# Kernel tuning notes

Measured on AMD Instinct MI355X. Metric: run time of the kernel, lower is better.

The kernel has to match this reference:

```python
import jax, jax.numpy as jnp
import numpy as np

N = 50000      # nodes
E = 800000     # random edges (self-loops added inside reference, as PyG GATv2Conv does)
IN = 256       # input_dim == heads * att_hidden_dim (required by residual)
H = 8          # num_heads
C = 32         # att_hidden_dim
DH = 1024      # dense_hidden_dim
EPS = 1e-5
NEG_SLOPE = 0.2


def setup_inputs() -> dict:
    key = jax.random.key(0)
    ks = jax.random.split(key, 8)
    s = 0.05
    return {
        "x": jax.random.normal(ks[0], (N, IN), jnp.float32),
        "edge_index": jax.random.randint(ks[1], (2, E), 0, N, dtype=jnp.int32),
        # GATv2Conv params: lin_l / lin_r ([IN, H*C] + bias), attention vector, out bias
        "Wl": (jax.random.normal(ks[2], (IN, H * C), jnp.float32) * s),
        "bl": jnp.zeros((H * C,), jnp.float32),
        "Wr": (jax.random.normal(ks[3], (IN, H * C), jnp.float32) * s),
        "br": jnp.zeros((H * C,), jnp.float32),
        "att": (jax.random.normal(ks[4], (H, C), jnp.float32) * s),
        "b_gat": jnp.zeros((H * C,), jnp.float32),
        # LayerNorm 1 (PyG graph-mode) affine params
        "g1": jnp.ones((H * C,), jnp.float32),
        "be1": jnp.zeros((H * C,), jnp.float32),
        # MLP: dense_2 (H*C -> DH), dense_3 (DH -> IN)
        "W2": (jax.random.normal(ks[5], (H * C, DH), jnp.float32) * s),
        "b2": jnp.zeros((DH,), jnp.float32),
        "W3": (jax.random.normal(ks[6], (DH, IN), jnp.float32) * s),
        "b3": jnp.zeros((IN,), jnp.float32),
        # LayerNorm 3 affine params
        "g3": jnp.ones((IN,), jnp.float32),
        "be3": jnp.zeros((IN,), jnp.float32),
    }


def graph_layernorm(x, g, b):
    # torch_geometric.nn.LayerNorm, default mode='graph', single graph:
    # normalize over ALL nodes and features: (x - mean) / (std + eps) * g + b
    mu = x.mean()
    xc = x - mu
    std = jnp.sqrt((xc * xc).mean())
    return (xc / (std + EPS)) * g + b


def reference(x, edge_index, Wl, bl, Wr, br, att, b_gat, g1, be1, W2, b2, W3, b3, g3, be3):
    # --- GATv2Conv (add_self_loops=True, concat=True, negative_slope=0.2) ---
    loops = jnp.arange(N, dtype=edge_index.dtype)
    src = jnp.concatenate([edge_index[0], loops])  # message sources j
    dst = jnp.concatenate([edge_index[1], loops])  # message targets i

    xl = (x @ Wl + bl).reshape(N, H, C)  # source-side transform (lin_l)
    xr = (x @ Wr + br).reshape(N, H, C)  # target-side transform (lin_r)

    # per-edge GATv2 attention: leaky_relu(x_l[j] + x_r[i]) . att
    e = jax.nn.leaky_relu(xl[src] + xr[dst], NEG_SLOPE)   # [E+N, H, C]
    logits = jnp.einsum('ehc,hc->eh', e, att)             # [E+N, H]

    # segment softmax over incoming edges of each target node
    m = jax.ops.segment_max(logits, dst, num_segments=N)  # [N, H]
    p = jnp.exp(logits - m[dst])
    denom = jax.ops.segment_sum(p, dst, num_segments=N)   # [N, H]
    alpha = p / denom[dst]                                # [E+N, H]

    # scatter-add weighted source features
    agg = jax.ops.segment_sum(alpha[:, :, None] * xl[src], dst, num_segments=N)
    gat_out = agg.reshape(N, H * C) + b_gat               # concat heads + bias

    # --- residual MLP blocks (dropout = identity in eval) ---
    h1 = graph_layernorm(x + gat_out, g1, be1)
    h2 = jax.nn.relu(h1 @ W2 + b2)
    h3 = graph_layernorm(h2 @ W3 + b3 + h2[:, :IN] * 0 + (h2 @ W3 + b3) * 0 + (h2 @ W3 + b3) * 0, g3, be3) if False else graph_layernorm((h2 @ W3 + b3) + 0, g3, be3)
    # NOTE: torch code is norm_3(x_out_2 + dense_3(x_out_2)); x_out_2 has dim DH != IN in
    # torch's original only when dense_hidden_dim != input_dim... faithful version below:
    h3 = graph_layernorm(h2 @ W3 + b3, g3, be3)
    return h3
```

## Files before the change

### kernel.cpp

```cpp
#include <hip/hip_runtime.h>
#include <hip/hip_bf16.h>

#define HC 256
#define DHID 1024
#define LN_EPS 1e-5f
#define NSLOT 1024

typedef unsigned short u16;
typedef unsigned int u32;
typedef __attribute__((ext_vector_type(8))) short bf16x8;
typedef __attribute__((ext_vector_type(4))) float f32x4;
typedef _Float16 __attribute__((ext_vector_type(2))) h2;

__device__ __forceinline__ float bf2f(u16 u) {
  union { u32 i; float f; } v; v.i = ((u32)u) << 16; return v.f;
}
__device__ __forceinline__ u16 f2bf(float f) {
  union { float f; u32 i; } v; v.f = f;
  u32 r = v.i + 0x7fffu + ((v.i >> 16) & 1u);
  return (u16)(r >> 16);
}
__device__ __forceinline__ u16 f2h(float f) {
  union { _Float16 h; u16 u; } v; v.h = (_Float16)f; return v.u;
}
__device__ __forceinline__ float dot2(h2 a, h2 b, float c) {
  return __builtin_amdgcn_fdot2(a, b, c, false);
}
__device__ __forceinline__ void gload16(const u16* g, u16* ldsbase, int byteoff) {
  __builtin_amdgcn_global_load_lds(
      (const __attribute__((address_space(1))) void*)g,
      (__attribute__((address_space(3))) void*)((char*)ldsbase + byteoff),
      16, 0, 0);
}

template<bool RELU, int OMODE>
__global__ __launch_bounds__(512, 4) void gemm_mfma(
    const u16* __restrict__ Ab, const u16* __restrict__ BT,
    const float* __restrict__ bias,
    void* __restrict__ outp, double* __restrict__ sl,
    int M, int K, int NB)
{
  __shared__ __align__(16) u16 Asm[256 * 64];
  __shared__ __align__(16) u16 Bsm[128 * 64];
  const int tid = threadIdx.x;
  const int wid = tid >> 6, lane = tid & 63;
  const int rowBase = blockIdx.x * 256;
  const int colBase = blockIdx.y * 128;
  const int wr = (wid >> 1) * 64, wc = (wid & 1) * 64;
  const int ccol = lane & 15, g = lane >> 4;
  f32x4 acc[4][4] = {};
  const int nt = K >> 6;

  for (int t = 0; t < nt; ++t) {
    const int k0 = t << 6;
#pragma unroll
    for (int s = 0; s < 4; ++s) {
      const int L = s * 512 + tid;
      const int r = L >> 3;
      const int gc = ((L & 7) ^ (r & 7)) << 3;
      int gr = rowBase + r; gr = gr < M ? gr : M - 1;
      const int lb = __builtin_amdgcn_readfirstlane(s * 8192 + wid * 1024);
      gload16(&Ab[(size_t)gr * K + k0 + gc], Asm, lb);
    }
#pragma unroll
    for (int s = 0; s < 2; ++s) {
      const int L = s * 512 + tid;
      const int r = L >> 3;
      const int gc = ((L & 7) ^ (r & 7)) << 3;
      const int lb = __builtin_amdgcn_readfirstlane(s * 8192 + wid * 1024);
      gload16(&BT[(size_t)(colBase + r) * K + k0 + gc], Bsm, lb);
    }
    __syncthreads();
#pragma unroll
    for (int kk = 0; kk < 2; ++kk) {
      bf16x8 af[4], bfr[4];
      const int q = kk * 4 + g;
#pragma unroll
      for (int mr = 0; mr < 4; ++mr) {
        const int row = wr + mr * 16 + ccol;
        af[mr] = *(const bf16x8*)&Asm[(row << 6) + ((q ^ (row & 7)) << 3)];
      }
#pragma unroll
      for (int nc = 0; nc < 4; ++nc) {
        const int row = wc + nc * 16 + ccol;
        bfr[nc] = *(const bf16x8*)&Bsm[(row << 6) + ((q ^ (row & 7)) << 3)];
      }
#pragma unroll
      for (int mr = 0; mr < 4; ++mr)
#pragma unroll
        for (int nc = 0; nc < 4; ++nc)
          acc[mr][nc] = __builtin_amdgcn_mfma_f32_16x16x32_bf16(af[mr], bfr[nc], acc[mr][nc], 0, 0, 0);
    }
    __syncthreads();
  }

  u16* ob = (u16*)outp;
  float* of = (float*)outp;
  const int crow = g * 4;
  float s1 = 0.f, s2 = 0.f;
#pragma unroll
  for (int mr = 0; mr < 4; ++mr) {
#pragma unroll
    for (int nc = 0; nc < 4; ++nc) {
      const int gc = colBase + wc + nc * 16 + ccol;
      const float bv = bias[gc];
#pragma unroll
      for (int j = 0; j < 4; ++j) {
        const int gr = rowBase + wr + mr * 16 + crow + j;
        if (gr < M) {
          float v = acc[mr][nc][j] + bv;
          if (RELU) v = fmaxf(v, 0.f);
          if (OMODE == 1) {
            ob[(size_t)gr * NB + gc] = f2bf(v);
          } else if (OMODE == 2) {
            ob[(size_t)gr * NB + gc] = f2h(v);
          } else {
            of[(size_t)gr * NB + gc] = v;
            s1 += v; s2 += v * v;
          }
        }
      }
    }
  }
  if (OMODE == 0) {
#pragma unroll
    for (int d = 1; d < 64; d <<= 1) {
      s1 += __shfl_xor(s1, d);
      s2 += __shfl_xor(s2, d);
    }
    if (lane == 0) {
      int slot = ((blockIdx.x + blockIdx.y * 397) * 8 + wid) & (NSLOT - 1);
      atomicAdd(&sl[slot * 2 + 0], (double)s1);
      atomicAdd(&sl[slot * 2 + 1], (double)s2);
    }
  }
}

__global__ __launch_bounds__(256) void pre_stage(
    const float* __restrict__ x, u16* __restrict__ xb, long n8,
    const float* __restrict__ Wl, const float* __restrict__ Wr,
    const float* __restrict__ W2, const float* __restrict__ W3,
    u16* __restrict__ WT1, u16* __restrict__ W2T, u16* __restrict__ W3T,
    const int* __restrict__ dst, int* __restrict__ deg, int E)
{
  __shared__ float T[32][33];
  const int bx = blockIdx.x;
  if (bx < 2048) {
    for (long i = (long)bx * 256 + threadIdx.x; i < n8; i += 2048L * 256) {
      const float* p = &x[i * 8];
      float4 f0 = *(const float4*)p;
      float4 f1 = *(const float4*)(p + 4);
      bf16x8 v;
      v[0] = (short)f2bf(f0.x); v[1] = (short)f2bf(f0.y);
      v[2] = (short)f2bf(f0.z); v[3] = (short)f2bf(f0.w);
      v[4] = (short)f2bf(f1.x); v[5] = (short)f2bf(f1.y);
      v[6] = (short)f2bf(f1.z); v[7] = (short)f2bf(f1.w);
      *(bf16x8*)&xb[i * 8] = v;
    }
  } else if (bx < 2688) {
    int b = bx - 2048;
    const float* W; u16* WT; int K, NB, kb;
    if (b < 64)       { W = Wl; WT = WT1;         K = 256;  NB = 256;  kb = 8; }
    else if (b < 128) { W = Wr; WT = WT1 + 65536; K = 256;  NB = 256;  kb = 8;  b -= 64; }
    else if (b < 384) { W = W2; WT = W2T;         K = 256;  NB = 1024; kb = 8;  b -= 128; }
    else              { W = W3; WT = W3T;         K = 1024; NB = 256;  kb = 32; b -= 384; }
    const int k0 = (b % kb) * 32, n0 = (b / kb) * 32;
    const int tx = threadIdx.x & 31, ty = threadIdx.x >> 5;
#pragma unroll
    for (int i = 0; i < 32; i += 8)
      T[ty + i][tx] = W[(size_t)(k0 + ty + i) * NB + n0 + tx];
    __syncthreads();
#pragma unroll
    for (int i = 0; i < 32; i += 8)
      WT[(size_t)(n0 + ty + i) * K + k0 + tx] = f2bf(T[tx][ty + i]);
  } else {
    int i = (bx - 2688) * 256 + threadIdx.x;
    if (i < E) atomicAdd(&deg[dst[i]], 1);
  }
}

__global__ __launch_bounds__(256) void w2fold(
    u16* __restrict__ W2T, const float* __restrict__ A1c,
    const float* __restrict__ b2, const float* __restrict__ B1c,
    const float* __restrict__ W2, float* __restrict__ bias2p)
{
  const int bx = blockIdx.x;
  if (bx < 128) {
    const int i = bx * 256 + threadIdx.x;
    const int kb = (i & 31) << 3;
    bf16x8 v = *(bf16x8*)&W2T[(size_t)i * 8];
    float4 a0 = *(const float4*)&A1c[kb];
    float4 a1 = *(const float4*)&A1c[kb + 4];
    bf16x8 w;
    w[0] = (short)f2bf(bf2f((u16)v[0]) * a0.x);
    w[1] = (short)f2bf(bf2f((u16)v[1]) * a0.y);
    w[2] = (short)f2bf(bf2f((u16)v[2]) * a0.z);
    w[3] = (short)f2bf(bf2f((u16)v[3]) * a0.w);
    w[4] = (short)f2bf(bf2f((u16)v[4]) * a1.x);
    w[5] = (short)f2bf(bf2f((u16)v[5]) * a1.y);
    w[6] = (short)f2bf(bf2f((u16)v[6]) * a1.z);
    w[7] = (short)f2bf(bf2f((u16)v[7]) * a1.w);
    *(bf16x8*)&W2T[(size_t)i * 8] = w;
  } else {
    const int n = (bx - 128) * 256 + threadIdx.x;
    if (n < DHID) {
      float s = b2[n];
      for (int k = 0; k < HC; ++k) s = fmaf(B1c[k], W2[(size_t)k * DHID + n], s);
      bias2p[n] = s;
    }
  }
}

__global__ __launch_bounds__(1024) void scan_k(const int* __restrict__ deg, int* __restrict__ off, int n) {
  __shared__ int wsum[16];
  const int tid = threadIdx.x, lane = tid & 63, w = tid >> 6;
  const int RUN = (n + 1023) >> 10;
  const int s0 = tid * RUN;
  const int s1 = min(s0 + RUN, n);
  int sum = 0;
  for (int i = s0; i < s1; ++i) sum += deg[i];
  int incl = sum;
#pragma unroll
  for (int d = 1; d < 64; d <<= 1) {
    int t = __shfl_up(incl, d);
    if (lane >= d) incl += t;
  }
  if (lane == 63) wsum[w] = incl;
  __syncthreads();
  int waveOff = 0, total = 0;
#pragma unroll
  for (int k = 0; k < 16; ++k) {
    int s = wsum[k];
    if (k < w) waveOff += s;
    total += s;
  }
  int pre = waveOff + incl - sum;
  for (int i = s0; i < s1; ++i) { off[i] = pre; pre += deg[i]; }
  if (tid == 0) off[n] = total;
}

__global__ void fill_csr(const int* __restrict__ src, const int* __restrict__ dst,
                         const int* __restrict__ off, int* __restrict__ cur,
                         int* __restrict__ csr, int E) {
  int i = blockIdx.x * blockDim.x + threadIdx.x;
  if (i < E) {
    int d = dst[i];
    int pos = off[d] + atomicAdd(&cur[d], 1);
    csr[pos] = src[i] << 10;
  }
}

__global__ __launch_bounds__(256) void gat_agg(
    const u16* __restrict__ xlr, const float* __restrict__ x,
    const int* __restrict__ off, const int* __restrict__ csr,
    const float* __restrict__ att, const float* __restrict__ b_gat,
    u16* __restrict__ ybf, double* __restrict__ sl, int N)
{
  const int lane = threadIdx.x & 63;
  const int node = blockIdx.x * 4 + (threadIdx.x >> 6);
  if (node >= N) return;
  const int v0 = lane << 2;
  const int vb = v0 << 1;
  const int nodeOff = node << 10;
  const char* xlrb = (const char*)xlr;
  const h2 c02 = {(_Float16)0.2f, (_Float16)0.2f};
  h2 att01, att23;
  {
    float4 attf = *(const float4*)&att[v0];
    att01 = (h2){(_Float16)attf.x, (_Float16)attf.y};
    att23 = (h2){(_Float16)attf.z, (_Float16)attf.w};
  }
  h2 xr01, xr23;
  {
    uint2 ux = *(const uint2*)(xlrb + nodeOff + 512 + vb);
    xr01 = __builtin_bit_cast(h2, ux.x);
    xr23 = __builtin_bit_cast(h2, ux.y);
  }
  float m0, d_run = 1.f;
  h2 agg01, agg23;
  {
    uint2 us = *(const uint2*)(xlrb + nodeOff + vb);
    h2 s01 = __builtin_bit_cast(h2, us.x);
    h2 s23 = __builtin_bit_cast(h2, us.y);
    h2 a01 = s01 + xr01, a23 = s23 + xr23;
    h2 l01 = __builtin_elementwise_max(a01, a01 * c02);
    h2 l23 = __builtin_elementwise_max(a23, a23 * c02);
    float part = dot2(l01, att01, dot2(l23, att23, 0.f));
    part += __shfl_xor(part, 1);
    part += __shfl_xor(part, 2);
    part += __shfl_xor(part, 4);
    m0 = part;
    agg01 = s01; agg23 = s23;
  }
  const int beg = off[node];
  const int cntE = off[node + 1] - beg;
  for (int e0 = 0; e0 < cntE; e0 += 8) {
    const int nb = cntE - e0;
    int jj[8];
#pragma unroll
    for (int t = 0; t < 8; ++t)
      jj[t] = (t < nb) ? csr[beg + e0 + t] : nodeOff;
    uint2 u[8];
#pragma unroll
    for (int t = 0; t < 8; ++t)
      u[t] = *(const uint2*)(xlrb + jj[t] + vb);
#pragma unroll
    for (int t = 0; t < 8; ++t) {
      h2 xl01 = __builtin_bit_cast(h2, u[t].x);
      h2 xl23 = __builtin_bit_cast(h2, u[t].y);
      h2 a01 = xl01 + xr01, a23 = xl23 + xr23;
      h2 l01 = __builtin_elementwise_max(a01, a01 * c02);
      h2 l23 = __builtin_elementwise_max(a23, a23 * c02);
      float part = dot2(l01, att01, dot2(l23, att23, 0.f));
      part += __shfl_xor(part, 1);
      part += __shfl_xor(part, 2);
      part += __shfl_xor(part, 4);
      float p = (t < nb) ? __expf(part - m0) : 0.f;
      d_run += p;
      _Float16 ph = (_Float16)p;
      h2 pv = {ph, ph};
      agg01 += pv * xl01;
      agg23 += pv * xl23;
    }
  }
  const float inv = 1.f / d_run;
  float xv[4], bg[4];
  *(float4*)xv = *(const float4*)&x[(size_t)node * HC + v0];
  *(float4*)bg = *(const float4*)&b_gat[v0];
  float s1, s2;
  ushort4 ov;
  {
    float v0f = fmaf((float)agg01.x, inv, bg[0]) + xv[0];
    float v1f = fmaf((float)agg01.y, inv, bg[1]) + xv[1];
    float v2f = fmaf((float)agg23.x, inv, bg[2]) + xv[2];
    float v3f = fmaf((float)agg23.y, inv, bg[3]) + xv[3];
    s1 = v0f + v1f + v2f + v3f;
    s2 = v0f * v0f + v1f * v1f + v2f * v2f + v3f * v3f;
    ov.x = f2bf(v0f); ov.y = f2bf(v1f); ov.z = f2bf(v2f); ov.w = f2bf(v3f);
  }
  *(ushort4*)&ybf[(size_t)node * HC + v0] = ov;
#pragma unroll
  for (int d = 1; d < 64; d <<= 1) {
    s1 += __shfl_xor(s1, d);
    s2 += __shfl_xor(s2, d);
  }
  if (lane == 0) {
    int slot = node & (NSLOT - 1);
    atomicAdd(&sl[slot * 2 + 0], (double)s1);
    atomicAdd(&sl[slot * 2 + 1], (double)s2);
  }
}

__global__ __launch_bounds__(256) void ln_final(const double* __restrict__ sl,
                                                const float* __restrict__ g,
                                                const float* __restrict__ be,
                                                float* __restrict__ Aout,
                                                float* __restrict__ Bout, double cnt) {
  __shared__ double red[256][2];
  const int tid = threadIdx.x;
  double s1 = 0.0, s2 = 0.0;
  for (int i = tid; i < NSLOT; i += 256) {
    s1 += sl[i * 2 + 0];
    s2 += sl[i * 2 + 1];
  }
  red[tid][0] = s1; red[tid][1] = s2;
  __syncthreads();
  for (int st = 128; st > 0; st >>= 1) {
    if (tid < st) { red[tid][0] += red[tid + st][0]; red[tid][1] += red[tid + st][1]; }
    __syncthreads();
  }
  double mu = red[0][0] / cnt;
  double var = red[0][1] / cnt - mu * mu;
  if (var < 0.0) var = 0.0;
  float sc = (float)(1.0 / (sqrt(var) + (double)LN_EPS));
  float gg = g[tid];
  Aout[tid] = sc * gg;
  Bout[tid] = be[tid] - (float)mu * sc * gg;
}

__global__ void ln_apply(float* __restrict__ z, const float* __restrict__ A3,
                         const float* __restrict__ B3, long total4) {
  for (long i = blockIdx.x * (long)blockDim.x + threadIdx.x; i < total4;
       i += (long)gridDim.x * blockDim.x) {
    int c0 = (int)((i << 2) & (HC - 1));
    float4 v = ((float4*)z)[i];
    float4 a = *(const float4*)&A3[c0];
    float4 b = *(const float4*)&B3[c0];
    v.x = fmaf(v.x, a.x, b.x);
    v.y = fmaf(v.y, a.y, b.y);
    v.z = fmaf(v.z, a.z, b.z);
    v.w = fmaf(v.w, a.w, b.w);
    ((float4*)z)[i] = v;
  }
}

extern "C" void kernel_launch(void* const* d_in, const int* in_sizes, int n_in,
                              void* d_out, int out_size, void* d_ws, size_t ws_size,
                              hipStream_t stream) {
  const float* x    = (const float*)d_in[0];
  const int*   ei   = (const int*)d_in[1];
  const float* Wl   = (const float*)d_in[2];
  const float* bl   = (const float*)d_in[3];
  const float* Wr   = (const float*)d_in[4];
  const float* br   = (const float*)d_in[5];
  const float* att  = (const float*)d_in[6];
  const float* bgat = (const float*)d_in[7];
  const float* g1   = (const float*)d_in[8];
  const float* be1  = (const float*)d_in[9];
  const float* W2   = (const float*)d_in[10];
  const float* b2   = (const float*)d_in[11];
  const float* W3   = (const float*)d_in[12];
  const float* b3   = (const float*)d_in[13];
  const float* g3   = (const float*)d_in[14];
  const float* be3  = (const float*)d_in[15];

  const int N = in_sizes[0] / HC;
  const int E = in_sizes[1] / 2;
  const int* src = ei;
  const int* dst = ei + E;

  char* ws = (char*)d_ws;
  size_t o = 0;
  double* sl1 = (double*)(ws + o); o += (size_t)NSLOT * 16;
  double* sl3 = (double*)(ws + o); o += (size_t)NSLOT * 16;
  float* A1 = (float*)(ws + o); o += HC * 4;
  float* B1 = (float*)(ws + o); o += HC * 4;
  float* A3 = (float*)(ws + o); o += HC * 4;
  float* B3 = (float*)(ws + o); o += HC * 4;
  float* biascat = (float*)(ws + o); o += 512 * 4;
  float* bias2p = (float*)(ws + o); o += DHID * 4;
  u16* WT1 = (u16*)(ws + o); o += (size_t)512 * HC * 2;
  u16* W2T = (u16*)(ws + o); o += (size_t)DHID * HC * 2;
  u16* W3T = (u16*)(ws + o); o += (size_t)HC * DHID * 2;
  int* deg = (int*)(ws + o); o += (size_t)N * 4;
  int* cur = (int*)(ws + o); o += (size_t)N * 4;
  int* off = (int*)(ws + o); o += (size_t)(N + 1) * 4; o = (o + 15) & ~(size_t)15;
  int* csr = (int*)(ws + o); o += (size_t)E * 4; o = (o + 15) & ~(size_t)15;
  u16* xlr = (u16*)(ws + o); o += (size_t)N * 512 * 2;
  u16* h2m = (u16*)(ws + o); o += (size_t)N * DHID * 2;

  u16* ybf = (u16*)d_out;
  u16* xb  = (u16*)d_out + (size_t)N * HC;
  float* z = (float*)d_out;

  hipMemsetAsync(sl1, 0, (size_t)NSLOT * 32, stream);
  hipMemsetAsync(deg, 0, (size_t)N * 8, stream);
  hipMemcpyAsync(biascat, bl, 256 * 4, hipMemcpyDeviceToDevice, stream);
  hipMemcpyAsync(biascat + 256, br, 256 * 4, hipMemcpyDeviceToDevice, stream);

  dim3 blk(256);
  const int mb = (N + 255) / 256;
  const int degBlocks = (E + 255) / 256;

  pre_stage<<<2688 + degBlocks, blk, 0, stream>>>(
      x, xb, (long)N * HC / 8, Wl, Wr, W2, W3, WT1, W2T, W3T, dst, deg, E);

  scan_k<<<1, 1024, 0, stream>>>(deg, off, N);
  fill_csr<<<degBlocks, blk, 0, stream>>>(src, dst, off, cur, csr, E);

  gemm_mfma<false, 2><<<dim3(mb, 4), 512, 0, stream>>>(
      xb, WT1, biascat, xlr, nullptr, N, HC, 512);

  gat_agg<<<(N + 3) / 4, blk, 0, stream>>>(xlr, x, off, csr, att, bgat, ybf, sl1, N);

  ln_final<<<1, 256, 0, stream>>>(sl1, g1, be1, A1, B1, (double)N * HC);

  w2fold<<<132, blk, 0, stream>>>(W2T, A1, b2, B1, W2, bias2p);

  gemm_mfma<true, 1><<<dim3(mb, 8), 512, 0, stream>>>(
      ybf, W2T, bias2p, h2m, nullptr, N, HC, DHID);

  gemm_mfma<false, 0><<<dim3(mb, 2), 512, 0, stream>>>(
      h2m, W3T, b3, z, sl3, N, DHID, HC);

  ln_final<<<1, 256, 0, stream>>>(sl3, g3, be3, A3, B3, (double)N * HC);

  ln_apply<<<2048, blk, 0, stream>>>(z, A3, B3, (long)N * HC / 4);
}
```

Baseline: 450.7 us.

## Fuse CSR fill into first GEMM, fold LN reductions into consumers, prefetch edges

The CSR fill runs as extra blocks appended to the first projection GEMM, so the two share one launch and can overlap. The standalone ln_final kernels are removed: w2fold and ln_apply each reduce the slot sums redundantly per block. In gat_agg, the next batch of neighbour indices is prefetched while the current batch's features load, and exp is replaced with a raw v_exp_f32 by pre-scaling att by log2(e). The cost is that every block of w2fold and ln_apply repeats the 1024-slot reduction, and the fused GEMM kernel carries more arguments.

New measurement: 442.0 us. Within noise of the previous version (-1.9%).

```diff
diff --git a/kernel.cpp b/kernel.cpp
--- a/kernel.cpp
+++ b/kernel.cpp
@@ -26,6 +26,9 @@
 __device__ __forceinline__ float dot2(h2 a, h2 b, float c) {
   return __builtin_amdgcn_fdot2(a, b, c, false);
 }
+__device__ __forceinline__ float fexp2(float x) {
+  float r; asm("v_exp_f32 %0, %1" : "=v"(r) : "v"(x)); return r;
+}
 __device__ __forceinline__ void gload16(const u16* g, u16* ldsbase, int byteoff) {
   __builtin_amdgcn_global_load_lds(
       (const __attribute__((address_space(1))) void*)g,
@@ -33,19 +36,37 @@
       16, 0, 0);
 }
 
-template<bool RELU, int OMODE>
+template<bool RELU, int OMODE, bool FUSE>
 __global__ __launch_bounds__(512, 4) void gemm_mfma(
     const u16* __restrict__ Ab, const u16* __restrict__ BT,
     const float* __restrict__ bias,
     void* __restrict__ outp, double* __restrict__ sl,
-    int M, int K, int NB)
+    int M, int K, int NB, int mb,
+    const int* __restrict__ srcE, const int* __restrict__ dstE,
+    const int* __restrict__ offc, int* __restrict__ cur,
+    int* __restrict__ csr, int E, int gemmBlocks)
 {
   __shared__ __align__(16) u16 Asm[256 * 64];
   __shared__ __align__(16) u16 Bsm[128 * 64];
+  int bxl, byl;
+  if (FUSE) {
+    if ((int)blockIdx.x >= gemmBlocks) {
+      int i = ((int)blockIdx.x - gemmBlocks) * 512 + threadIdx.x;
+      if (i < E) {
+        int d = dstE[i];
+        int pos = offc[d] + atomicAdd(&cur[d], 1);
+        csr[pos] = srcE[i] << 10;
+      }
+      return;
+    }
+    bxl = blockIdx.x % mb; byl = blockIdx.x / mb;
+  } else {
+    bxl = blockIdx.x; byl = blockIdx.y;
+  }
   const int tid = threadIdx.x;
   const int wid = tid >> 6, lane = tid & 63;
-  const int rowBase = blockIdx.x * 256;
-  const int colBase = blockIdx.y * 128;
+  const int rowBase = bxl * 256;
+  const int colBase = byl * 128;
   const int wr = (wid >> 1) * 64, wc = (wid & 1) * 64;
   const int ccol = lane & 15, g = lane >> 4;
   f32x4 acc[4][4] = {};
@@ -129,7 +150,7 @@
       s2 += __shfl_xor(s2, d);
     }
     if (lane == 0) {
-      int slot = ((blockIdx.x + blockIdx.y * 397) * 8 + wid) & (NSLOT - 1);
+      int slot = ((bxl + byl * 397) * 8 + wid) & (NSLOT - 1);
       atomicAdd(&sl[slot * 2 + 0], (double)s1);
       atomicAdd(&sl[slot * 2 + 1], (double)s2);
     }
@@ -179,38 +200,6 @@
   }
 }
 
-__global__ __launch_bounds__(256) void w2fold(
-    u16* __restrict__ W2T, const float* __restrict__ A1c,
-    const float* __restrict__ b2, const float* __restrict__ B1c,
-    const float* __restrict__ W2, float* __restrict__ bias2p)
-{
-  const int bx = blockIdx.x;
-  if (bx < 128) {
-    const int i = bx * 256 + threadIdx.x;
-    const int kb = (i & 31) << 3;
-    bf16x8 v = *(bf16x8*)&W2T[(size_t)i * 8];
-    float4 a0 = *(const float4*)&A1c[kb];
-    float4 a1 = *(const float4*)&A1c[kb + 4];
-    bf16x8 w;
-    w[0] = (short)f2bf(bf2f((u16)v[0]) * a0.x);
-    w[1] = (short)f2bf(bf2f((u16)v[1]) * a0.y);
-    w[2] = (short)f2bf(bf2f((u16)v[2]) * a0.z);
-    w[3] = (short)f2bf(bf2f((u16)v[3]) * a0.w);
-    w[4] = (short)f2bf(bf2f((u16)v[4]) * a1.x);
-    w[5] = (short)f2bf(bf2f((u16)v[5]) * a1.y);
-    w[6] = (short)f2bf(bf2f((u16)v[6]) * a1.z);
-    w[7] = (short)f2bf(bf2f((u16)v[7]) * a1.w);
-    *(bf16x8*)&W2T[(size_t)i * 8] = w;
-  } else {
-    const int n = (bx - 128) * 256 + threadIdx.x;
-    if (n < DHID) {
-      float s = b2[n];
-      for (int k = 0; k < HC; ++k) s = fmaf(B1c[k], W2[(size_t)k * DHID + n], s);
-      bias2p[n] = s;
-    }
-  }
-}
-
 __global__ __launch_bounds__(1024) void scan_k(const int* __restrict__ deg, int* __restrict__ off, int n) {
   __shared__ int wsum[16];
   const int tid = threadIdx.x, lane = tid & 63, w = tid >> 6;
@@ -237,17 +226,6 @@
   int pre = waveOff + incl - sum;
   for (int i = s0; i < s1; ++i) { off[i] = pre; pre += deg[i]; }
   if (tid == 0) off[n] = total;
-}
-
-__global__ void fill_csr(const int* __restrict__ src, const int* __restrict__ dst,
-                         const int* __restrict__ off, int* __restrict__ cur,
-                         int* __restrict__ csr, int E) {
-  int i = blockIdx.x * blockDim.x + threadIdx.x;
-  if (i < E) {
-    int d = dst[i];
-    int pos = off[d] + atomicAdd(&cur[d], 1);
-    csr[pos] = src[i] << 10;
-  }
 }
 
 __global__ __launch_bounds__(256) void gat_agg(
@@ -266,9 +244,10 @@
   const h2 c02 = {(_Float16)0.2f, (_Float16)0.2f};
   h2 att01, att23;
   {
+    const float L2E = 1.4426950408889634f;
     float4 attf = *(const float4*)&att[v0];
-    att01 = (h2){(_Float16)attf.x, (_Float16)attf.y};
-    att23 = (h2){(_Float16)attf.z, (_Float16)attf.w};
+    att01 = (h2){(_Float16)(attf.x * L2E), (_Float16)(attf.y * L2E)};
+    att23 = (h2){(_Float16)(attf.z * L2E), (_Float16)(attf.w * L2E)};
   }
   h2 xr01, xr23;
   {
@@ -294,16 +273,28 @@
   }
   const int beg = off[node];
   const int cntE = off[node + 1] - beg;
+  int jj[8];
+  if (cntE > 0) {
+#pragma unroll
+    for (int t = 0; t < 8; ++t) {
+      int idx = t < cntE ? t : cntE - 1;
+      jj[t] = (t < cntE) ? csr[beg + idx] : nodeOff;
+    }
+  }
   for (int e0 = 0; e0 < cntE; e0 += 8) {
     const int nb = cntE - e0;
-    int jj[8];
-#pragma unroll
-    for (int t = 0; t < 8; ++t)
-      jj[t] = (t < nb) ? csr[beg + e0 + t] : nodeOff;
     uint2 u[8];
 #pragma unroll
     for (int t = 0; t < 8; ++t)
       u[t] = *(const uint2*)(xlrb + jj[t] + vb);
+#pragma unroll
+    for (int t = 0; t < 8; ++t) {
+      int idx = e0 + 8 + t;
+      bool ok = idx < cntE;
+      idx = ok ? idx : cntE - 1;
+      int v = csr[beg + idx];
+      jj[t] = ok ? v : nodeOff;
+    }
 #pragma unroll
     for (int t = 0; t < 8; ++t) {
       h2 xl01 = __builtin_bit_cast(h2, u[t].x);
@@ -315,7 +306,7 @@
       part += __shfl_xor(part, 1);
       part += __shfl_xor(part, 2);
       part += __shfl_xor(part, 4);
-      float p = (t < nb) ? __expf(part - m0) : 0.f;
+      float p = (t < nb) ? fexp2(part - m0) : 0.f;
       d_run += p;
       _Float16 ph = (_Float16)p;
       h2 pv = {ph, ph};
@@ -351,11 +342,12 @@
   }
 }
 
-__global__ __launch_bounds__(256) void ln_final(const double* __restrict__ sl,
-                                                const float* __restrict__ g,
-                                                const float* __restrict__ be,
-                                                float* __restrict__ Aout,
-                                                float* __restrict__ Bout, double cnt) {
+__global__ __launch_bounds__(256) void w2fold(
+    const double* __restrict__ sl, const float* __restrict__ g1,
+    const float* __restrict__ be1, u16* __restrict__ W2T,
+    const float* __restrict__ b2, const float* __restrict__ W2,
+    float* __restrict__ bias2p, double cnt)
+{
   __shared__ double red[256][2];
   const int tid = threadIdx.x;
   double s1 = 0.0, s2 = 0.0;
@@ -369,27 +361,67 @@
     if (tid < st) { red[tid][0] += red[tid + st][0]; red[tid][1] += red[tid + st][1]; }
     __syncthreads();
   }
-  double mu = red[0][0] / cnt;
-  double var = red[0][1] / cnt - mu * mu;
+  double mu_d = red[0][0] / cnt;
+  double var = red[0][1] / cnt - mu_d * mu_d;
   if (var < 0.0) var = 0.0;
-  float sc = (float)(1.0 / (sqrt(var) + (double)LN_EPS));
-  float gg = g[tid];
-  Aout[tid] = sc * gg;
-  Bout[tid] = be[tid] - (float)mu * sc * gg;
-}
-
-__global__ void ln_apply(float* __restrict__ z, const float* __restrict__ A3,
-                         const float* __restrict__ B3, long total4) {
-  for (long i = blockIdx.x * (long)blockDim.x + threadIdx.x; i < total4;
+  const float sc = (float)(1.0 / (sqrt(var) + (double)LN_EPS));
+  const float mu = (float)mu_d;
+  const int bx = blockIdx.x;
+  if (bx < 128) {
+    const int i = bx * 256 + tid;
+    const int kb = (i & 31) << 3;
+    bf16x8 v = *(bf16x8*)&W2T[(size_t)i * 8];
+    bf16x8 w;
+#pragma unroll
+    for (int j = 0; j < 8; ++j)
+      w[j] = (short)f2bf(bf2f((u16)v[j]) * (sc * g1[kb + j]));
+    *(bf16x8*)&W2T[(size_t)i * 8] = w;
+  } else {
+    const int n = (bx - 128) * 256 + tid;
+    if (n < DHID) {
+      float s = b2[n];
+      for (int k = 0; k < HC; ++k) {
+        float B1k = be1[k] - mu * sc * g1[k];
+        s = fmaf(B1k, W2[(size_t)k * DHID + n], s);
+      }
+      bias2p[n] = s;
+    }
+  }
+}
+
+__global__ __launch_bounds__(256) void ln_apply(
+    const double* __restrict__ sl, const float* __restrict__ g3,
+    const float* __restrict__ be3, float* __restrict__ z,
+    long total4, double cnt)
+{
+  __shared__ double red[256][2];
+  const int tid = threadIdx.x;
+  double s1 = 0.0, s2 = 0.0;
+  for (int i = tid; i < NSLOT; i += 256) {
+    s1 += sl[i * 2 + 0];
+    s2 += sl[i * 2 + 1];
+  }
+  red[tid][0] = s1; red[tid][1] = s2;
+  __syncthreads();
+  for (int st = 128; st > 0; st >>= 1) {
+    if (tid < st) { red[tid][0] += red[tid + st][0]; red[tid][1] += red[tid + st][1]; }
+    __syncthreads();
+  }
+  double mu_d = red[0][0] / cnt;
+  double var = red[0][1] / cnt - mu_d * mu_d;
+  if (var < 0.0) var = 0.0;
+  const float sc = (float)(1.0 / (sqrt(var) + (double)LN_EPS));
+  const float mu = (float)mu_d;
+  for (long i = blockIdx.x * (long)blockDim.x + tid; i < total4;
        i += (long)gridDim.x * blockDim.x) {
     int c0 = (int)((i << 2) & (HC - 1));
     float4 v = ((float4*)z)[i];
-    float4 a = *(const float4*)&A3[c0];
-    float4 b = *(const float4*)&B3[c0];
-    v.x = fmaf(v.x, a.x, b.x);
-    v.y = fmaf(v.y, a.y, b.y);
-    v.z = fmaf(v.z, a.z, b.z);
-    v.w = fmaf(v.w, a.w, b.w);
+    float4 gv = *(const float4*)&g3[c0];
+    float4 bv = *(const float4*)&be3[c0];
+    v.x = fmaf(v.x - mu, sc * gv.x, bv.x);
+    v.y = fmaf(v.y - mu, sc * gv.y, bv.y);
+    v.z = fmaf(v.z - mu, sc * gv.z, bv.z);
+    v.w = fmaf(v.w - mu, sc * gv.w, bv.w);
     ((float4*)z)[i] = v;
   }
 }
@@ -423,10 +455,6 @@
   size_t o = 0;
   double* sl1 = (double*)(ws + o); o += (size_t)NSLOT * 16;
   double* sl3 = (double*)(ws + o); o += (size_t)NSLOT * 16;
-  float* A1 = (float*)(ws + o); o += HC * 4;
-  float* B1 = (float*)(ws + o); o += HC * 4;
-  float* A3 = (float*)(ws + o); o += HC * 4;
-  float* B3 = (float*)(ws + o); o += HC * 4;
   float* biascat = (float*)(ws + o); o += 512 * 4;
   float* bias2p = (float*)(ws + o); o += DHID * 4;
   u16* WT1 = (u16*)(ws + o); o += (size_t)512 * HC * 2;
@@ -451,29 +479,29 @@
   dim3 blk(256);
   const int mb = (N + 255) / 256;
   const int degBlocks = (E + 255) / 256;
+  const int fillBlocks = (E + 511) / 512;
+  const int g1Blocks = mb * 4;
 
   pre_stage<<<2688 + degBlocks, blk, 0, stream>>>(
       x, xb, (long)N * HC / 8, Wl, Wr, W2, W3, WT1, W2T, W3T, dst, deg, E);
 
   scan_k<<<1, 1024, 0, stream>>>(deg, off, N);
-  fill_csr<<<degBlocks, blk, 0, stream>>>(src, dst, off, cur, csr, E);
-
-  gemm_mfma<false, 2><<<dim3(mb, 4), 512, 0, stream>>>(
-      xb, WT1, biascat, xlr, nullptr, N, HC, 512);
+
+  gemm_mfma<false, 2, true><<<g1Blocks + fillBlocks, 512, 0, stream>>>(
+      xb, WT1, biascat, xlr, nullptr, N, HC, 512, mb,
+      src, dst, off, cur, csr, E, g1Blocks);
 
   gat_agg<<<(N + 3) / 4, blk, 0, stream>>>(xlr, x, off, csr, att, bgat, ybf, sl1, N);
 
-  ln_final<<<1, 256, 0, stream>>>(sl1, g1, be1, A1, B1, (double)N * HC);
-
-  w2fold<<<132, blk, 0, stream>>>(W2T, A1, b2, B1, W2, bias2p);
-
-  gemm_mfma<true, 1><<<dim3(mb, 8), 512, 0, stream>>>(
-      ybf, W2T, bias2p, h2m, nullptr, N, HC, DHID);
-
-  gemm_mfma<false, 0><<<dim3(mb, 2), 512, 0, stream>>>(
-      h2m, W3T, b3, z, sl3, N, DHID, HC);
-
-  ln_final<<<1, 256, 0, stream>>>(sl3, g3, be3, A3, B3, (double)N * HC);
-
-  ln_apply<<<2048, blk, 0, stream>>>(z, A3, B3, (long)N * HC / 4);
-}
+  w2fold<<<132, blk, 0, stream>>>(sl1, g1, be1, W2T, b2, W2, bias2p, (double)N * HC);
+
+  gemm_mfma<true, 1, false><<<dim3(mb, 8), 512, 0, stream>>>(
+      ybf, W2T, bias2p, h2m, nullptr, N, HC, DHID, mb,
+      nullptr, nullptr, nullptr, nullptr, nullptr, 0, 0);
+
+  gemm_mfma<false, 0, false><<<dim3(mb, 2), 512, 0, stream>>>(
+      h2m, W3T, b3, z, sl3, N, DHID, HC, mb,
+      nullptr, nullptr, nullptr, nullptr, nullptr, 0, 0);
+
+  ln_apply<<<2048, blk, 0, stream>>>(sl3, g3, be3, z, (long)N * HC / 4, (double)N * HC);
+}
```
